# Kernel tuning notes

Measured on AMD Instinct MI355X. Metric: run time of the kernel, lower is better.

The kernel has to match this reference:

```python
import jax, jax.numpy as jnp
import numpy as np
from jax import lax

USER_NUM = 100000
COMP_NUM = 50000
ENTITY_NUM = USER_NUM + COMP_NUM + 2  # 150002
N_ACTIVE = USER_NUM + COMP_NUM        # 150000 valid graph nodes
REL_NUM = 200
D = 128
T = 12        # timesteps
E = 250000    # edges per timestep
S = 20000     # seed (LSTM-updated) nodes per timestep
B = 1024      # user batch
USER_ID_MAX = 99999


def setup_inputs() -> dict:
    key = jax.random.key(0)
    ks = jax.random.split(key, 16)
    ent_emb = jax.random.normal(ks[0], (ENTITY_NUM, D), jnp.float32) * 0.02
    c0_emb = jax.random.normal(ks[1], (ENTITY_NUM, D), jnp.float32) * 0.02
    rel_emb = jax.random.normal(ks[2], (REL_NUM, D), jnp.float32) * 0.02
    W_ih = jax.random.normal(ks[3], (4 * D, D), jnp.float32) * (1.0 / np.sqrt(D))
    W_hh = jax.random.normal(ks[4], (4 * D, D), jnp.float32) * (1.0 / np.sqrt(D))
    b_ih = jax.random.normal(ks[5], (4 * D,), jnp.float32) * 0.01
    b_hh = jax.random.normal(ks[6], (4 * D,), jnp.float32) * 0.01
    src = jax.random.randint(ks[7], (T, E), 0, N_ACTIVE, jnp.int32)
    dst = jax.random.randint(ks[8], (T, E), 0, N_ACTIVE, jnp.int32)
    rel_idx = jax.random.randint(ks[9], (T, E), 0, REL_NUM, jnp.int32)
    # unique seed nodes per timestep (scatter targets must not collide)
    seed_keys = jax.random.split(ks[10], T)
    seed_idx = jax.vmap(lambda k: jax.random.permutation(k, N_ACTIVE)[:S])(seed_keys).astype(jnp.int32)
    user_batch = jax.random.randint(ks[11], (B,), 0, USER_NUM, jnp.int32)
    comp_target = jax.random.randint(ks[12], (B,), 0, COMP_NUM, jnp.int32)
    job_target = jax.random.randint(ks[13], (B,), 0, REL_NUM // 2, jnp.int32)
    return {"ent_emb": ent_emb, "c0_emb": c0_emb, "rel_emb": rel_emb,
            "W_ih": W_ih, "W_hh": W_hh, "b_ih": b_ih, "b_hh": b_hh,
            "src": src, "dst": dst, "rel_idx": rel_idx, "seed_idx": seed_idx,
            "user_batch": user_batch, "comp_target": comp_target, "job_target": job_target}


def reference(ent_emb, c0_emb, rel_emb, W_ih, W_hh, b_ih, b_hh,
              src, dst, rel_idx, seed_idx, user_batch, comp_target, job_target):
    def step(carry, xs):
        h, c = carry                       # [N, D] node_emb / cx
        s, d, r, seed = xs
        # msg_GCN: m = src_node_emb * rel_emb[rel]; reduce_GCN: mean over mailbox
        m = h[s] * rel_emb[r]              # [E, D]
        msum = jax.ops.segment_sum(m, d, num_segments=ENTITY_NUM)
        cnt = jax.ops.segment_sum(jnp.ones((E,), h.dtype), d, num_segments=ENTITY_NUM)
        x = h + msum / jnp.maximum(cnt, 1.0)[:, None]   # update_node: node_emb + node_emb2
        # LSTMCell on seed nodes only (input = aggregated emb, state = pre-agg emb, cx)
        xi, hp, cp = x[seed], h[seed], c[seed]          # [S, D]
        gates = xi @ W_ih.T + b_ih + hp @ W_hh.T + b_hh  # [S, 4D]
        ig, fg, gg, og = jnp.split(gates, 4, axis=-1)
        cn = jax.nn.sigmoid(fg) * cp + jax.nn.sigmoid(ig) * jnp.tanh(gg)
        hn = jax.nn.sigmoid(og) * jnp.tanh(cn)
        return (x.at[seed].set(hn), c.at[seed].set(cn)), None

    (h, _c), _ = lax.scan(step, (ent_emb, c0_emb), (src, dst, rel_idx, seed_idx))

    u = h[user_batch]                                   # [B, D] user time embeddings
    # company softmax-CE (logsumexp over all companies)
    tc = ent_emb[comp_target + USER_ID_MAX + 1]
    all_c = ent_emb[USER_ID_MAX + 1: USER_ID_MAX + 1 + COMP_NUM]  # [COMP_NUM, D]
    pos_c = jnp.sum(u * tc, axis=1)
    comp_loss = -jnp.sum(pos_c - jax.nn.logsumexp(u @ all_c.T, axis=1))
    # job (relation) softmax-CE over rel_num // 2 jobs
    tj = rel_emb[job_target]
    all_j = rel_emb[: REL_NUM // 2]
    pos_j = jnp.sum(u * tj, axis=1)
    job_loss = -jnp.sum(pos_j - jax.nn.logsumexp(u @ all_j.T, axis=1))
    return jnp.stack([comp_loss, job_loss])
```

## Files before the change

kernel.cpp:

```cpp
#include <hip/hip_runtime.h>
#include <math.h>

typedef __attribute__((ext_vector_type(8))) short short8;
typedef __attribute__((ext_vector_type(8))) unsigned short u16x8;
typedef __attribute__((ext_vector_type(4))) float f32x4;
typedef __attribute__((ext_vector_type(2))) float f32x2;
typedef long i64;

#define USER_NUM_  100000
#define COMP_NUM_  50000
#define EN         150002
#define REL_NUM_   200
#define DD         128
#define TT         12
#define EE         250000
#define SS         20000
#define BB         1024
#define PPART      125
#define TILES_PP   25
#define NB         37
#define BSH        12
#define CHUNK      4096
#define NCH        62

__device__ inline unsigned short f2bf(float f) {
    unsigned u = __float_as_uint(f);
    unsigned r = (u + 0x7fffu + ((u >> 16) & 1u)) >> 16;
    return (unsigned short)r;
}

__device__ inline float bf2f(unsigned short u) {
    return __uint_as_float((unsigned)u << 16);
}

__device__ inline void fp8x8_to_f(uint2 u, float f[8]) {
    f32x2 a = __builtin_amdgcn_cvt_pk_f32_fp8((int)u.x, false);
    f32x2 b = __builtin_amdgcn_cvt_pk_f32_fp8((int)u.x, true);
    f32x2 c = __builtin_amdgcn_cvt_pk_f32_fp8((int)u.y, false);
    f32x2 d = __builtin_amdgcn_cvt_pk_f32_fp8((int)u.y, true);
    f[0] = a[0]; f[1] = a[1]; f[2] = b[0]; f[3] = b[1];
    f[4] = c[0]; f[5] = c[1]; f[6] = d[0]; f[7] = d[1];
}

__device__ inline unsigned fp8x4_pack(float f0, float f1, float f2, float f3) {
    int v = __builtin_amdgcn_cvt_pk_fp8_f32(f0, f1, 0, false);
    v = __builtin_amdgcn_cvt_pk_fp8_f32(f2, f3, v, true);
    return (unsigned)v;
}

__device__ inline unsigned char f_to_fp8(float f) {
    return (unsigned char)(__builtin_amdgcn_cvt_pk_fp8_f32(f, f, 0, false) & 0xff);
}

__device__ inline float fp8_to_f(unsigned char b) {
    return __builtin_amdgcn_cvt_f32_fp8((int)b, 0);
}

__device__ inline float sigmoidf_(float x) { return 1.f / (1.f + __expf(-x)); }

__device__ inline void lse_push(float v, float& m, float& s) {
    if (v <= m) { s += __expf(v - m); }
    else { s = s * __expf(m - v) + 1.f; m = v; }
}

__device__ inline void lse_merge(float& M, float& S, float M2, float S2) {
    float Mn = fmaxf(M, M2);
    S = S * __expf(M - Mn) + S2 * __expf(M2 - Mn);
    M = Mn;
}

__global__ __launch_bounds__(256) void packBF_k(const float* __restrict__ src, ushort4* __restrict__ dst, int n4) {
    int i = blockIdx.x * 256 + threadIdx.x;
    if (i >= n4) return;
    float4 v = ((const float4*)src)[i];
    ushort4 o;
    o.x = f2bf(v.x); o.y = f2bf(v.y); o.z = f2bf(v.z); o.w = f2bf(v.w);
    dst[i] = o;
}

__global__ __launch_bounds__(256) void packF8_k(const float* __restrict__ src, unsigned* __restrict__ dst, int n4) {
    int i = blockIdx.x * 256 + threadIdx.x;
    if (i >= n4) return;
    float4 v = ((const float4*)src)[i];
    dst[i] = fp8x4_pack(v.x, v.y, v.z, v.w);
}

__global__ __launch_bounds__(256) void zero_i32_k(int* __restrict__ p, int n) {
    int i = blockIdx.x * 256 + threadIdx.x;
    if (i < n) p[i] = 0;
}

__global__ __launch_bounds__(256) void prepW_k(const float* __restrict__ Wih, const float* __restrict__ Whh,
                                               const float* __restrict__ bih, const float* __restrict__ bhh,
                                               unsigned char* __restrict__ Wt8, float* __restrict__ bsum) {
    int n = blockIdx.x;
    int k = threadIdx.x;
    float v = (k < 128) ? Wih[n * 128 + k] : Whh[n * 128 + (k - 128)];
    Wt8[n * 256 + k] = f_to_fp8(v);
    if (k == 0) bsum[n] = bih[n] + bhh[n];
}

__global__ __launch_bounds__(256) void binA_k(const int* __restrict__ dst, int* __restrict__ bcnt,
                                              int t0) {
    int slot = blockIdx.y;
    int tid = threadIdx.x;
    int c0 = blockIdx.x * CHUNK;
    int w = tid >> 6;
    __shared__ int lcnt[4][NB];
    for (int i = tid; i < 4 * NB; i += 256) ((int*)lcnt)[i] = 0;
    __syncthreads();
#pragma unroll
    for (int i = 0; i < 16; ++i) {
        int e = c0 + i * 256 + tid;
        if (e < EE) {
            int d = __builtin_nontemporal_load(&dst[(size_t)(t0 + slot) * EE + e]);
            atomicAdd(&lcnt[w][d >> BSH], 1);
        }
    }
    __syncthreads();
    if (tid < NB)
        atomicAdd(&bcnt[slot * NB + tid], lcnt[0][tid] + lcnt[1][tid] + lcnt[2][tid] + lcnt[3][tid]);
}

__global__ __launch_bounds__(64) void binScan_k(const int* __restrict__ bcnt, int* __restrict__ bbase,
                                                int* __restrict__ bcur, int nt) {
    int slot = threadIdx.x;
    if (slot >= nt) return;
    int b = 0;
    for (int c = 0; c < NB; ++c) {
        bbase[slot * (NB + 1) + c] = b;
        bcur[slot * NB + c] = b;
        b += bcnt[slot * NB + c];
    }
    bbase[slot * (NB + 1) + NB] = b;
}

__global__ __launch_bounds__(256) void binB_k(const int* __restrict__ src, const int* __restrict__ dst,
                                              const int* __restrict__ rel, int* __restrict__ bcur,
                                              int2* __restrict__ bucketed, int t0) {
    int slot = blockIdx.y;
    int tid = threadIdx.x;
    int c0 = blockIdx.x * CHUNK;
    __shared__ int lcnt[NB], lbase[NB], gbase[NB], lcur[NB];
    __shared__ int2 stage[CHUNK];
    if (tid < NB) lcnt[tid] = 0;
    __syncthreads();

    int myb[16]; int2 myv[16];
#pragma unroll
    for (int i = 0; i < 16; ++i) {
        int e = c0 + i * 256 + tid;
        if (e < EE) {
            size_t gi = (size_t)(t0 + slot) * EE + e;
            int d = __builtin_nontemporal_load(&dst[gi]);
            int s = __builtin_nontemporal_load(&src[gi]);
            int r = __builtin_nontemporal_load(&rel[gi]);
            myb[i] = d >> BSH;
            myv[i] = make_int2(d, s | (r << 18));
            atomicAdd(&lcnt[myb[i]], 1);
        } else myb[i] = -1;
    }
    __syncthreads();
    if (tid == 0) {
        int b = 0;
        for (int c = 0; c < NB; ++c) { lbase[c] = b; b += lcnt[c]; }
    }
    __syncthreads();
    if (tid < NB) {
        gbase[tid] = (lcnt[tid] > 0) ? atomicAdd(&bcur[slot * NB + tid], lcnt[tid]) : 0;
        lcur[tid] = lbase[tid];
    }
    __syncthreads();
#pragma unroll
    for (int i = 0; i < 16; ++i) {
        if (myb[i] >= 0) {
            int p = atomicAdd(&lcur[myb[i]], 1);
            stage[p] = myv[i];
        }
    }
    __syncthreads();
    int w = tid >> 6, lane = tid & 63;
    int2* bout = bucketed + (size_t)slot * EE;
    for (int b = w; b < NB; b += 4) {
        int cnt = lcnt[b], lb = lbase[b], gb = gbase[b];
        for (int j = lane; j < cnt; j += 64)
            bout[gb + j] = stage[lb + j];
    }
}

__global__ __launch_bounds__(256) void histC_k(const int2* __restrict__ bucketed,
                                               const int* __restrict__ bbase,
                                               int* __restrict__ startp) {
    int b = blockIdx.x, slot = blockIdx.y;
    int tid = threadIdx.x;
    int base_ent = b << BSH;
    int nloc = EN - base_ent; if (nloc > 4096) nloc = 4096;
    __shared__ int lcnt[4096];
    __shared__ int tsum[256];
    for (int i = tid; i < 4096; i += 256) lcnt[i] = 0;
    __syncthreads();
    int e0 = bbase[slot * (NB + 1) + b], e1 = bbase[slot * (NB + 1) + b + 1];
    for (int e = e0 + tid; e < e1; e += 256) {
        int2 ed = bucketed[(size_t)slot * EE + e];
        atomicAdd(&lcnt[ed.x - base_ent], 1);
    }
    __syncthreads();
    int base16 = tid * 16;
    int s = 0;
#pragma unroll
    for (int k = 0; k < 16; ++k) s += lcnt[base16 + k];
    tsum[tid] = s;
    __syncthreads();
#pragma unroll
    for (int o = 1; o < 256; o <<= 1) {
        int x = (tid >= o) ? tsum[tid - o] : 0;
        __syncthreads();
        tsum[tid] += x;
        __syncthreads();
    }
    int run = e0 + tsum[tid] - s;
#pragma unroll
    for (int k = 0; k < 16; ++k) {
        int c = lcnt[base16 + k];
        lcnt[base16 + k] = run;
        run += c;
    }
    __syncthreads();
    for (int i = tid; i < nloc; i += 256) startp[(size_t)slot * EN + base_ent + i] = lcnt[i];
}

__global__ __launch_bounds__(256) void scatB_k(const int2* __restrict__ bucketed,
                                               const int* __restrict__ bbase,
                                               int* __restrict__ startp, int* __restrict__ pairs) {
    int b = blockIdx.x, slot = blockIdx.y;
    int tid = threadIdx.x;
    int base_ent = b << BSH;
    int nloc = EN - base_ent; if (nloc > 4096) nloc = 4096;
    __shared__ int lcur[4096];
    for (int i = tid; i < nloc; i += 256) lcur[i] = startp[(size_t)slot * EN + base_ent + i];
    __syncthreads();
    int e0 = bbase[slot * (NB + 1) + b], e1 = bbase[slot * (NB + 1) + b + 1];
    for (int e = e0 + tid; e < e1; e += 256) {
        int2 ed = bucketed[(size_t)slot * EE + e];
        int pos = atomicAdd(&lcur[ed.x - base_ent], 1);
        pairs[(size_t)slot * EE + pos] = ed.y;
    }
    __syncthreads();
    for (int i = tid; i < nloc; i += 256) startp[(size_t)slot * EN + base_ent + i] = lcur[i];
}

__global__ __launch_bounds__(256) void agg_k(const unsigned char* __restrict__ hold,
                                             unsigned char* __restrict__ hnew,
                                             const unsigned short* __restrict__ Rbf,
                                             const int* __restrict__ endp_all,
                                             const int* __restrict__ pairs, int slot) {
    int tid = threadIdx.x;
    int d = blockIdx.x * 16 + (tid >> 4);
    int l = tid & 15;
    if (d >= EN) return;
    const int* endp = endp_all + (size_t)slot * EN;
    int e0 = (d > 0) ? endp[d - 1] : 0;
    int e1 = endp[d];
    const int* pp = pairs + (size_t)slot * EE;
    float acc[8];
#pragma unroll
    for (int j = 0; j < 8; ++j) acc[j] = 0.f;
    int e = e0;
    for (; e + 2 <= e1; e += 2) {
        int pk0 = pp[e], pk1 = pp[e + 1];
        uint2 h0 = *(const uint2*)(hold + (size_t)(pk0 & 0x3FFFF) * DD + l * 8);
        u16x8 r0 = *(const u16x8*)(Rbf + (size_t)(pk0 >> 18) * DD + l * 8);
        uint2 h1 = *(const uint2*)(hold + (size_t)(pk1 & 0x3FFFF) * DD + l * 8);
        u16x8 r1 = *(const u16x8*)(Rbf + (size_t)(pk1 >> 18) * DD + l * 8);
        float hf0[8], hf1[8];
        fp8x8_to_f(h0, hf0);
        fp8x8_to_f(h1, hf1);
#pragma unroll
        for (int j = 0; j < 8; ++j)
            acc[j] = fmaf(hf1[j], bf2f(r1[j]), fmaf(hf0[j], bf2f(r0[j]), acc[j]));
    }
    if (e < e1) {
        int pk0 = pp[e];
        uint2 h0 = *(const uint2*)(hold + (size_t)(pk0 & 0x3FFFF) * DD + l * 8);
        u16x8 r0 = *(const u16x8*)(Rbf + (size_t)(pk0 >> 18) * DD + l * 8);
        float hf0[8];
        fp8x8_to_f(h0, hf0);
#pragma unroll
        for (int j = 0; j < 8; ++j)
            acc[j] = fmaf(hf0[j], bf2f(r0[j]), acc[j]);
    }
    uint2 hd = *(const uint2*)(hold + (size_t)d * DD + l * 8);
    float hdf[8];
    fp8x8_to_f(hd, hdf);
    int c = e1 - e0;
    float inv = (c > 0) ? 1.f / (float)c : 0.f;
    float o[8];
#pragma unroll
    for (int j = 0; j < 8; ++j) o[j] = fmaf(acc[j], inv, hdf[j]);
    uint2 ov;
    ov.x = fp8x4_pack(o[0], o[1], o[2], o[3]);
    ov.y = fp8x4_pack(o[4], o[5], o[6], o[7]);
    *(uint2*)(hnew + (size_t)d * DD + l * 8) = ov;
}

__global__ __launch_bounds__(256) void lstm_k(const unsigned char* __restrict__ hold,
                                              unsigned char* __restrict__ hnew,
                                              unsigned short* __restrict__ cbuf,
                                              const unsigned char* __restrict__ Wt8,
                                              const float* __restrict__ bsum, const int* __restrict__ seed) {
    int w = threadIdx.x >> 6;
    int lane = threadIdx.x & 63;
    int lrow = lane & 15, lhi = lane >> 4;
    int m0 = blockIdx.x * 32;
    int w32 = w * 32;

    const unsigned char* pxi[2];
    const unsigned char* php[2];
#pragma unroll
    for (int mi = 0; mi < 2; ++mi) {
        int m = m0 + mi * 16 + lrow;
        int sd = seed[m];
        pxi[mi] = hnew + (size_t)sd * DD;
        php[mi] = hold + (size_t)sd * DD;
    }

    f32x4 acc[2][4][2];
#pragma unroll
    for (int mi = 0; mi < 2; ++mi)
#pragma unroll
        for (int g = 0; g < 4; ++g)
#pragma unroll
            for (int s = 0; s < 2; ++s)
                acc[mi][g][s] = (f32x4){0.f, 0.f, 0.f, 0.f};

#pragma unroll
    for (int kk = 0; kk < 8; ++kk) {
        int klane = kk * 32 + lhi * 8;
        i64 af[2];
#pragma unroll
        for (int mi = 0; mi < 2; ++mi) {
            const unsigned char* p = (klane < 128) ? (pxi[mi] + klane) : (php[mi] + (klane - 128));
            af[mi] = *(const i64*)p;
        }
#pragma unroll
        for (int g = 0; g < 4; ++g)
#pragma unroll
            for (int s = 0; s < 2; ++s) {
                int col = g * 128 + w32 + s * 16 + lrow;
                i64 bf = *(const i64*)(Wt8 + (size_t)col * 256 + klane);
                acc[0][g][s] = __builtin_amdgcn_mfma_f32_16x16x32_fp8_fp8(af[0], bf, acc[0][g][s], 0, 0, 0);
                acc[1][g][s] = __builtin_amdgcn_mfma_f32_16x16x32_fp8_fp8(af[1], bf, acc[1][g][s], 0, 0, 0);
            }
    }

    __syncthreads();

#pragma unroll
    for (int mi = 0; mi < 2; ++mi) {
#pragma unroll
        for (int r = 0; r < 4; ++r) {
            int m = m0 + mi * 16 + lhi * 4 + r;
            int sd = seed[m];
#pragma unroll
            for (int s = 0; s < 2; ++s) {
                int d = w32 + s * 16 + lrow;
                float ig = acc[mi][0][s][r] + bsum[d];
                float fg = acc[mi][1][s][r] + bsum[128 + d];
                float gg = acc[mi][2][s][r] + bsum[256 + d];
                float og = acc[mi][3][s][r] + bsum[384 + d];
                float cp = bf2f(cbuf[(size_t)sd * DD + d]);
                float cn = sigmoidf_(fg) * cp + sigmoidf_(ig) * tanhf(gg);
                float hn = sigmoidf_(og) * tanhf(cn);
                cbuf[(size_t)sd * DD + d] = f2bf(cn);
                hnew[(size_t)sd * DD + d] = f_to_fp8(hn);
            }
        }
    }
}

__global__ __launch_bounds__(256) void packU_k(const unsigned char* __restrict__ hfin, const int* __restrict__ ub,
                                               short* __restrict__ Ubf) {
    int i = blockIdx.x * 256 + threadIdx.x;
    if (i >= BB * DD) return;
    int u = i >> 7, k = i & 127;
    Ubf[i] = (short)f2bf(fp8_to_f(hfin[(size_t)ub[u] * DD + k]));
}

__global__ __launch_bounds__(256) void comp_mfma_k(const short* __restrict__ Ubf, const short* __restrict__ Cbf,
                                                   float* __restrict__ partm, float* __restrict__ parts) {
    int tid = threadIdx.x;
    int w = tid >> 6, lane = tid & 63;
    int lrow = lane & 15, lhi = lane >> 4;
    int ubase = blockIdx.x * 128 + w * 32;
    int p = blockIdx.y;

    __shared__ __align__(16) short ct[2][16][136];

    short8 a[2][4];
#pragma unroll
    for (int s2 = 0; s2 < 2; ++s2)
#pragma unroll
        for (int kc = 0; kc < 4; ++kc)
            a[s2][kc] = *(const short8*)(Ubf + (size_t)(ubase + s2 * 16 + lrow) * DD + kc * 32 + lhi * 8);

    float s[2][4];
#pragma unroll
    for (int s2 = 0; s2 < 2; ++s2)
#pragma unroll
        for (int r = 0; r < 4; ++r) s[s2][r] = 0.f;

    int c0 = p * TILES_PP * 16;
    int srow = tid >> 4, scol = (tid & 15) * 8;
    {
        short8 v = *(const short8*)(Cbf + (size_t)(c0 + srow) * DD + scol);
        *(short8*)&ct[0][srow][scol] = v;
    }

    for (int tile = 0; tile < TILES_PP; ++tile) {
        int cur = tile & 1;
        short8 pf;
        bool hn = (tile + 1 < TILES_PP);
        if (hn)
            pf = *(const short8*)(Cbf + (size_t)(c0 + (tile + 1) * 16 + srow) * DD + scol);
        __syncthreads();
        if (hn) *(short8*)&ct[cur ^ 1][srow][scol] = pf;

        f32x4 acc0 = {0.f, 0.f, 0.f, 0.f};
        f32x4 acc1 = {0.f, 0.f, 0.f, 0.f};
#pragma unroll
        for (int kc = 0; kc < 4; ++kc) {
            short8 b = *(const short8*)&ct[cur][lrow][kc * 32 + lhi * 8];
            acc0 = __builtin_amdgcn_mfma_f32_16x16x32_bf16(a[0][kc], b, acc0, 0, 0, 0);
            acc1 = __builtin_amdgcn_mfma_f32_16x16x32_bf16(a[1][kc], b, acc1, 0, 0, 0);
        }
#pragma unroll
        for (int r = 0; r < 4; ++r) {
            s[0][r] += __expf(acc0[r]);
            s[1][r] += __expf(acc1[r]);
        }
    }

#pragma unroll
    for (int s2 = 0; s2 < 2; ++s2)
#pragma unroll
        for (int r = 0; r < 4; ++r) {
            float S = s[s2][r];
#pragma unroll
            for (int o = 1; o < 16; o <<= 1)
                S += __shfl_xor(S, o, 64);
            if (lrow == 0) {
                int u = ubase + s2 * 16 + lhi * 4 + r;
                partm[(size_t)u * PPART + p] = 0.f;
                parts[(size_t)u * PPART + p] = S;
            }
        }
}

__global__ __launch_bounds__(256) void finish2_k(const unsigned char* __restrict__ hfin,
                                                 const float* __restrict__ ent,
                                                 const float* __restrict__ rel, const int* __restrict__ ub,
                                                 const int* __restrict__ ct, const int* __restrict__ jt,
                                                 const float* __restrict__ partm, const float* __restrict__ parts,
                                                 float* __restrict__ out) {
    __shared__ float s_u[4][128];
    int w = threadIdx.x >> 6, lane = threadIdx.x & 63;
    int u = blockIdx.x * 4 + w;

    const unsigned char* up = hfin + (size_t)ub[u] * DD;
    float u0 = fp8_to_f(up[lane]), u1 = fp8_to_f(up[lane + 64]);
    s_u[w][lane] = u0;
    s_u[w][lane + 64] = u1;

    const float* tcp = ent + (size_t)(USER_NUM_ + ct[u]) * DD;
    float pc = u0 * tcp[lane] + u1 * tcp[lane + 64];
    const float* tjp = rel + (size_t)jt[u] * DD;
    float pj = u0 * tjp[lane] + u1 * tjp[lane + 64];
#pragma unroll
    for (int o = 1; o < 64; o <<= 1) {
        pc += __shfl_xor(pc, o, 64);
        pj += __shfl_xor(pj, o, 64);
    }

    float M = partm[(size_t)u * PPART + lane];
    float S = parts[(size_t)u * PPART + lane];
    if (lane + 64 < PPART)
        lse_merge(M, S, partm[(size_t)u * PPART + lane + 64], parts[(size_t)u * PPART + lane + 64]);
#pragma unroll
    for (int o = 1; o < 64; o <<= 1) {
        float M2 = __shfl_xor(M, o, 64);
        float S2 = __shfl_xor(S, o, 64);
        lse_merge(M, S, M2, S2);
    }
    float lse_c = M + logf(S);

    int j1 = lane, j2 = lane + 64;
    bool v2 = j2 < (REL_NUM_ / 2);
    const float* r1 = rel + (size_t)j1 * DD;
    const float* r2 = rel + (size_t)(v2 ? j2 : 0) * DD;
    float d1 = 0.f, d2 = 0.f;
#pragma unroll 16
    for (int k = 0; k < DD; ++k) {
        float uk = s_u[w][k];
        d1 = fmaf(uk, r1[k], d1);
        d2 = fmaf(uk, r2[k], d2);
    }
    float Mj = d1, Sj = 1.f;
    if (v2) lse_push(d2, Mj, Sj);
#pragma unroll
    for (int o = 1; o < 64; o <<= 1) {
        float M2 = __shfl_xor(Mj, o, 64);
        float S2 = __shfl_xor(Sj, o, 64);
        lse_merge(Mj, Sj, M2, S2);
    }
    float lse_j = Mj + logf(Sj);

    if (lane == 0) {
        atomicAdd(&out[0], lse_c - pc);
        atomicAdd(&out[1], lse_j - pj);
    }
}

static inline size_t rup(size_t x) { return (x + 255) & ~(size_t)255; }

extern "C" void kernel_launch(void* const* d_in, const int* in_sizes, int n_in,
                              void* d_out, int out_size, void* d_ws, size_t ws_size,
                              hipStream_t stream) {
    const float* ent_emb = (const float*)d_in[0];
    const float* c0_emb  = (const float*)d_in[1];
    const float* rel_emb = (const float*)d_in[2];
    const float* W_ih    = (const float*)d_in[3];
    const float* W_hh    = (const float*)d_in[4];
    const float* b_ih    = (const float*)d_in[5];
    const float* b_hh    = (const float*)d_in[6];
    const int* src       = (const int*)d_in[7];
    const int* dst       = (const int*)d_in[8];
    const int* rel_idx   = (const int*)d_in[9];
    const int* seed_idx  = (const int*)d_in[10];
    const int* ubatch    = (const int*)d_in[11];
    const int* ctarg     = (const int*)d_in[12];
    const int* jtarg     = (const int*)d_in[13];
    float* out = (float*)d_out;

    const size_t HB8 = rup((size_t)EN * DD);
    const size_t HBH = rup((size_t)EN * DD * 2);

    char* base = (char*)d_ws;
    unsigned char* h0   = (unsigned char*)base;
    unsigned char* h1   = (unsigned char*)(base + HB8);
    unsigned short* cbuf = (unsigned short*)(base + 2 * HB8);

    int* startp; int* pairs; int2* bucketed; int* bcnt; int* bbase; int* bcur;
    unsigned char* Wt8; float* bsumv; unsigned short* Rbf;
    auto place = [&](int NT) -> size_t {
        size_t o = 2 * HB8 + HBH;
        startp   = (int*)(base + o);  o += rup((size_t)NT * EN * 4);
        pairs    = (int*)(base + o);  o += rup((size_t)NT * EE * 4);
        bucketed = (int2*)(base + o); o += rup((size_t)NT * EE * 8);
        bcnt     = (int*)(base + o);  o += rup((size_t)NT * NB * 4);
        bbase    = (int*)(base + o);  o += rup((size_t)NT * (NB + 1) * 4);
        bcur     = (int*)(base + o);  o += rup((size_t)NT * NB * 4);
        Wt8      = (unsigned char*)(base + o); o += rup(512 * 256);
        bsumv    = (float*)(base + o); o += rup(512 * 4);
        Rbf      = (unsigned short*)(base + o); o += rup((size_t)REL_NUM_ * DD * 2);
        return o;
    };

    const int cands[6] = {12, 6, 4, 3, 2, 1};
    int NT = 1;
    for (int i = 0; i < 6; ++i) {
        if (place(cands[i]) <= ws_size) { NT = cands[i]; break; }
    }
    place(NT);

    char* q = (char*)cbuf;
    short* Cbf = (short*)q;            q += rup((size_t)COMP_NUM_ * DD * 2);
    short* Ubf = (short*)q;            q += rup((size_t)BB * DD * 2);
    float* partm = (float*)q;          q += rup((size_t)BB * PPART * 4);
    float* parts = (float*)q;

    hipMemsetAsync(d_out, 0, 2 * sizeof(float), stream);

    const int n4 = EN * DD / 4;
    const int gcpy = (n4 + 255) / 256;

    prepW_k<<<512, 256, 0, stream>>>(W_ih, W_hh, b_ih, b_hh, Wt8, bsumv);
    packF8_k<<<gcpy, 256, 0, stream>>>(ent_emb, (unsigned*)h0, n4);
    packBF_k<<<gcpy, 256, 0, stream>>>(c0_emb, (ushort4*)cbuf, n4);
    packBF_k<<<(REL_NUM_ * DD / 4 + 255) / 256, 256, 0, stream>>>(rel_emb, (ushort4*)Rbf, REL_NUM_ * DD / 4);

    auto build = [&](int t0, int nt) {
        zero_i32_k<<<(nt * NB + 255) / 256, 256, 0, stream>>>(bcnt, nt * NB);
        binA_k<<<dim3(NCH, nt), 256, 0, stream>>>(dst, bcnt, t0);
        binScan_k<<<1, 64, 0, stream>>>(bcnt, bbase, bcur, nt);
        binB_k<<<dim3(NCH, nt), 256, 0, stream>>>(src, dst, rel_idx, bcur, bucketed, t0);
        histC_k<<<dim3(NB, nt), 256, 0, stream>>>(bucketed, bbase, startp);
        scatB_k<<<dim3(NB, nt), 256, 0, stream>>>(bucketed, bbase, startp, pairs);
    };

    unsigned char* hold = h0;
    unsigned char* hnew = h1;
    const int gagg = (EN + 15) / 16;

    for (int b0 = 0; b0 < TT; b0 += NT) {
        int nb = (TT - b0 < NT) ? (TT - b0) : NT;
        build(b0, nb);
        for (int k = 0; k < nb; ++k) {
            int t = b0 + k;
            agg_k<<<gagg, 256, 0, stream>>>(hold, hnew, Rbf, startp, pairs, k);
            lstm_k<<<SS / 32, 256, 0, stream>>>(hold, hnew, cbuf, Wt8, bsumv, seed_idx + (size_t)t * SS);
            unsigned char* tmp = hold; hold = hnew; hnew = tmp;
        }
    }

    packBF_k<<<(COMP_NUM_ * DD / 4 + 255) / 256, 256, 0, stream>>>(ent_emb + (size_t)USER_NUM_ * DD,
                                                                   (ushort4*)Cbf, COMP_NUM_ * DD / 4);
    packU_k<<<(BB * DD + 255) / 256, 256, 0, stream>>>(hold, ubatch, Ubf);
    comp_mfma_k<<<dim3(BB / 128, PPART), 256, 0, stream>>>(Ubf, Cbf, partm, parts);
    finish2_k<<<BB / 4, 256, 0, stream>>>(hold, ent_emb, rel_emb, ubatch, ctarg, jtarg,
                                          partm, parts, out);
}
```

Baseline: 858.0 us.

## Fuse histogram and scatter CSR kernels; halve LSTM rows per block

```diff
diff --git a/kernel.cpp b/kernel.cpp
--- a/kernel.cpp
+++ b/kernel.cpp
@@ -188,9 +188,9 @@
     }
 }
 
-__global__ __launch_bounds__(256) void histC_k(const int2* __restrict__ bucketed,
-                                               const int* __restrict__ bbase,
-                                               int* __restrict__ startp) {
+__global__ __launch_bounds__(256) void histscat_k(const int2* __restrict__ bucketed,
+                                                  const int* __restrict__ bbase,
+                                                  int* __restrict__ startp, int* __restrict__ pairs) {
     int b = blockIdx.x, slot = blockIdx.y;
     int tid = threadIdx.x;
     int base_ent = b << BSH;
@@ -200,10 +200,9 @@
     for (int i = tid; i < 4096; i += 256) lcnt[i] = 0;
     __syncthreads();
     int e0 = bbase[slot * (NB + 1) + b], e1 = bbase[slot * (NB + 1) + b + 1];
-    for (int e = e0 + tid; e < e1; e += 256) {
-        int2 ed = bucketed[(size_t)slot * EE + e];
-        atomicAdd(&lcnt[ed.x - base_ent], 1);
-    }
+    const int2* bin = bucketed + (size_t)slot * EE;
+    for (int e = e0 + tid; e < e1; e += 256)
+        atomicAdd(&lcnt[bin[e].x - base_ent], 1);
     __syncthreads();
     int base16 = tid * 16;
     int s = 0;
@@ -226,27 +225,15 @@
         run += c;
     }
     __syncthreads();
-    for (int i = tid; i < nloc; i += 256) startp[(size_t)slot * EN + base_ent + i] = lcnt[i];
-}
-
-__global__ __launch_bounds__(256) void scatB_k(const int2* __restrict__ bucketed,
-                                               const int* __restrict__ bbase,
-                                               int* __restrict__ startp, int* __restrict__ pairs) {
-    int b = blockIdx.x, slot = blockIdx.y;
-    int tid = threadIdx.x;
-    int base_ent = b << BSH;
-    int nloc = EN - base_ent; if (nloc > 4096) nloc = 4096;
-    __shared__ int lcur[4096];
-    for (int i = tid; i < nloc; i += 256) lcur[i] = startp[(size_t)slot * EN + base_ent + i];
-    __syncthreads();
-    int e0 = bbase[slot * (NB + 1) + b], e1 = bbase[slot * (NB + 1) + b + 1];
+    int* pout = pairs + (size_t)slot * EE;
     for (int e = e0 + tid; e < e1; e += 256) {
-        int2 ed = bucketed[(size_t)slot * EE + e];
-        int pos = atomicAdd(&lcur[ed.x - base_ent], 1);
-        pairs[(size_t)slot * EE + pos] = ed.y;
-    }
-    __syncthreads();
-    for (int i = tid; i < nloc; i += 256) startp[(size_t)slot * EN + base_ent + i] = lcur[i];
+        int2 ed = bin[e];
+        int pos = atomicAdd(&lcnt[ed.x - base_ent], 1);
+        pout[pos] = ed.y;
+    }
+    __syncthreads();
+    for (int i = tid; i < nloc; i += 256)
+        startp[(size_t)slot * EN + base_ent + i] = lcnt[i];
 }
 
 __global__ __launch_bounds__(256) void agg_k(const unsigned char* __restrict__ hold,
@@ -311,69 +298,53 @@
     int w = threadIdx.x >> 6;
     int lane = threadIdx.x & 63;
     int lrow = lane & 15, lhi = lane >> 4;
-    int m0 = blockIdx.x * 32;
+    int m0 = blockIdx.x * 16;
     int w32 = w * 32;
 
-    const unsigned char* pxi[2];
-    const unsigned char* php[2];
-#pragma unroll
-    for (int mi = 0; mi < 2; ++mi) {
-        int m = m0 + mi * 16 + lrow;
-        int sd = seed[m];
-        pxi[mi] = hnew + (size_t)sd * DD;
-        php[mi] = hold + (size_t)sd * DD;
-    }
-
-    f32x4 acc[2][4][2];
-#pragma unroll
-    for (int mi = 0; mi < 2; ++mi)
-#pragma unroll
-        for (int g = 0; g < 4; ++g)
-#pragma unroll
-            for (int s = 0; s < 2; ++s)
-                acc[mi][g][s] = (f32x4){0.f, 0.f, 0.f, 0.f};
+    int sd_row = seed[m0 + lrow];
+    const unsigned char* pxi = hnew + (size_t)sd_row * DD;
+    const unsigned char* php = hold + (size_t)sd_row * DD;
+
+    f32x4 acc[4][2];
+#pragma unroll
+    for (int g = 0; g < 4; ++g)
+#pragma unroll
+        for (int s = 0; s < 2; ++s)
+            acc[g][s] = (f32x4){0.f, 0.f, 0.f, 0.f};
 
 #pragma unroll
     for (int kk = 0; kk < 8; ++kk) {
         int klane = kk * 32 + lhi * 8;
-        i64 af[2];
-#pragma unroll
-        for (int mi = 0; mi < 2; ++mi) {
-            const unsigned char* p = (klane < 128) ? (pxi[mi] + klane) : (php[mi] + (klane - 128));
-            af[mi] = *(const i64*)p;
-        }
+        const unsigned char* p = (klane < 128) ? (pxi + klane) : (php + (klane - 128));
+        i64 af = *(const i64*)p;
 #pragma unroll
         for (int g = 0; g < 4; ++g)
 #pragma unroll
             for (int s = 0; s < 2; ++s) {
                 int col = g * 128 + w32 + s * 16 + lrow;
                 i64 bf = *(const i64*)(Wt8 + (size_t)col * 256 + klane);
-                acc[0][g][s] = __builtin_amdgcn_mfma_f32_16x16x32_fp8_fp8(af[0], bf, acc[0][g][s], 0, 0, 0);
-                acc[1][g][s] = __builtin_amdgcn_mfma_f32_16x16x32_fp8_fp8(af[1], bf, acc[1][g][s], 0, 0, 0);
+                acc[g][s] = __builtin_amdgcn_mfma_f32_16x16x32_fp8_fp8(af, bf, acc[g][s], 0, 0, 0);
             }
     }
 
     __syncthreads();
 
 #pragma unroll
-    for (int mi = 0; mi < 2; ++mi) {
-#pragma unroll
-        for (int r = 0; r < 4; ++r) {
-            int m = m0 + mi * 16 + lhi * 4 + r;
-            int sd = seed[m];
-#pragma unroll
-            for (int s = 0; s < 2; ++s) {
-                int d = w32 + s * 16 + lrow;
-                float ig = acc[mi][0][s][r] + bsum[d];
-                float fg = acc[mi][1][s][r] + bsum[128 + d];
-                float gg = acc[mi][2][s][r] + bsum[256 + d];
-                float og = acc[mi][3][s][r] + bsum[384 + d];
-                float cp = bf2f(cbuf[(size_t)sd * DD + d]);
-                float cn = sigmoidf_(fg) * cp + sigmoidf_(ig) * tanhf(gg);
-                float hn = sigmoidf_(og) * tanhf(cn);
-                cbuf[(size_t)sd * DD + d] = f2bf(cn);
-                hnew[(size_t)sd * DD + d] = f_to_fp8(hn);
-            }
+    for (int r = 0; r < 4; ++r) {
+        int m = m0 + lhi * 4 + r;
+        int sd = seed[m];
+#pragma unroll
+        for (int s = 0; s < 2; ++s) {
+            int d = w32 + s * 16 + lrow;
+            float ig = acc[0][s][r] + bsum[d];
+            float fg = acc[1][s][r] + bsum[128 + d];
+            float gg = acc[2][s][r] + bsum[256 + d];
+            float og = acc[3][s][r] + bsum[384 + d];
+            float cp = bf2f(cbuf[(size_t)sd * DD + d]);
+            float cn = sigmoidf_(fg) * cp + sigmoidf_(ig) * tanhf(gg);
+            float hn = sigmoidf_(og) * tanhf(cn);
+            cbuf[(size_t)sd * DD + d] = f2bf(cn);
+            hnew[(size_t)sd * DD + d] = f_to_fp8(hn);
         }
     }
 }
@@ -593,8 +564,7 @@
         binA_k<<<dim3(NCH, nt), 256, 0, stream>>>(dst, bcnt, t0);
         binScan_k<<<1, 64, 0, stream>>>(bcnt, bbase, bcur, nt);
         binB_k<<<dim3(NCH, nt), 256, 0, stream>>>(src, dst, rel_idx, bcur, bucketed, t0);
-        histC_k<<<dim3(NB, nt), 256, 0, stream>>>(bucketed, bbase, startp);
-        scatB_k<<<dim3(NB, nt), 256, 0, stream>>>(bucketed, bbase, startp, pairs);
+        histscat_k<<<dim3(NB, nt), 256, 0, stream>>>(bucketed, bbase, startp, pairs);
     };
 
     unsigned char* hold = h0;
@@ -607,7 +577,7 @@
         for (int k = 0; k < nb; ++k) {
             int t = b0 + k;
             agg_k<<<gagg, 256, 0, stream>>>(hold, hnew, Rbf, startp, pairs, k);
-            lstm_k<<<SS / 32, 256, 0, stream>>>(hold, hnew, cbuf, Wt8, bsumv, seed_idx + (size_t)t * SS);
+            lstm_k<<<SS / 16, 256, 0, stream>>>(hold, hnew, cbuf, Wt8, bsumv, seed_idx + (size_t)t * SS);
             unsigned char* tmp = hold; hold = hnew; hnew = tmp;
         }
     }
```

After: 961.7 us. 1.12x slower.
